# Optimization experiments

Measured on AMD Instinct MI355X. Metric: run time of the kernel, lower is better.

The kernel has to match this reference:

```python
import jax, jax.numpy as jnp
import numpy as np
from jax import lax

N_NODES = 4096
WINDOW = 288
SLIDE = 12
ENC_STEPS = 12
DEC_STEPS = 12
HID = 64
EMB = 64
PRED = 12
C1, C2 = 32, 64
KSZ, STR = 10, 2
OUT_LEN = 66  # ((288-10)//2+1 -> 140; (140-10)//2+1 -> 66)
EPS = 1e-5


def _conv1d(x, w, b, stride):
    # x: [N, Cin, L], w: [Cout, Cin, K]
    y = lax.conv_general_dilated(x, w, (stride,), 'VALID',
                                 dimension_numbers=('NCH', 'OIH', 'NCH'))
    return y + b[None, :, None]


def _bn(x, g, b):
    # BatchNorm1d training-mode stats over (batch, length) per channel
    m = x.mean(axis=(0, 2), keepdims=True)
    v = x.var(axis=(0, 2), keepdims=True)
    return (x - m) * jax.lax.rsqrt(v + EPS) * g[None, :, None] + b[None, :, None]


def _embed(x, conv1_w, conv1_b, conv2_w, conv2_b, bn1_g, bn1_b, bn2_g, bn2_b,
           fcconv_w, fcconv_b, fc_w, fc_b):
    # x: [N, WINDOW] -> [N, EMB]
    x = x[:, None, :]                                   # [N,1,W]
    x = _bn(jax.nn.relu(_conv1d(x, conv1_w, conv1_b, STR)), bn1_g, bn1_b)
    x = _bn(jax.nn.relu(_conv1d(x, conv2_w, conv2_b, STR)), bn2_g, bn2_b)
    x = jax.nn.relu(_conv1d(x, fcconv_w, fcconv_b, 1))  # [N,1,OUT_LEN]
    x = jnp.einsum('ncl,le->nce', x, fc_w) + fc_b       # [N,1,EMB]
    # NOTE: original code calls F.relu(x) but discards the result -> no relu here
    return x[:, 0, :]


def _gconv(x, adj, W, b):
    # diffusion conv: [x, A x, 2A(Ax) - x] (K=2, includes identity term)
    x1 = adj @ x
    x2 = 2.0 * (adj @ x1) - x
    return jnp.concatenate([x, x1, x2], axis=-1) @ W + b


def _dcgru_cell(x, h, adj, Wg, bg, Wc, bc):
    ru = jax.nn.sigmoid(_gconv(jnp.concatenate([x, h], -1), adj, Wg, bg))
    r, u = jnp.split(ru, 2, axis=-1)
    c = jnp.tanh(_gconv(jnp.concatenate([x, r * h], -1), adj, Wc, bc))
    return u * h + (1.0 - u) * c


def setup_inputs() -> dict:
    key = jax.random.key(0)
    ks = jax.random.split(key, 20)
    n_mat = 3  # K+1 diffusion matrices
    gin = (EMB + HID) * n_mat
    inp = {
        'inputs': jax.random.normal(ks[0], (N_NODES, (ENC_STEPS + DEC_STEPS - 1) * SLIDE + WINDOW), jnp.float32),
        'targets': jax.random.normal(ks[1], (N_NODES, DEC_STEPS * PRED), jnp.float32),
        'conv1_w': jax.random.normal(ks[3], (C1, 1, KSZ), jnp.float32) * 0.1,
        'conv1_b': jnp.zeros((C1,), jnp.float32),
        'conv2_w': jax.random.normal(ks[4], (C2, C1, KSZ), jnp.float32) * 0.1,
        'conv2_b': jnp.zeros((C2,), jnp.float32),
        'bn1_g': jnp.ones((C1,), jnp.float32), 'bn1_b': jnp.zeros((C1,), jnp.float32),
        'bn2_g': jnp.ones((C2,), jnp.float32), 'bn2_b': jnp.zeros((C2,), jnp.float32),
        'fcconv_w': jax.random.normal(ks[5], (1, C2, 1), jnp.float32) * 0.1,
        'fcconv_b': jnp.zeros((1,), jnp.float32),
        'fc_w': jax.random.normal(ks[6], (OUT_LEN, EMB), jnp.float32) * (1.0 / np.sqrt(OUT_LEN)),
        'fc_b': jnp.zeros((EMB,), jnp.float32),
        'enc_Wg': jax.random.normal(ks[7], (gin, 2 * HID), jnp.float32) * (1.0 / np.sqrt(gin)),
        'enc_bg': jnp.ones((2 * HID,), jnp.float32),
        'enc_Wc': jax.random.normal(ks[8], (gin, HID), jnp.float32) * (1.0 / np.sqrt(gin)),
        'enc_bc': jnp.zeros((HID,), jnp.float32),
        'dec_Wg': jax.random.normal(ks[9], (gin, 2 * HID), jnp.float32) * (1.0 / np.sqrt(gin)),
        'dec_bg': jnp.ones((2 * HID,), jnp.float32),
        'dec_Wc': jax.random.normal(ks[10], (gin, HID), jnp.float32) * (1.0 / np.sqrt(gin)),
        'dec_bc': jnp.zeros((HID,), jnp.float32),
        'pred_w': jax.random.normal(ks[11], (HID, PRED), jnp.float32) * (1.0 / np.sqrt(HID)),
        'pred_b': jnp.full((PRED,), 0.1, jnp.float32),
    }
    a = jax.random.uniform(ks[2], (N_NODES, N_NODES), jnp.float32)
    inp['adj'] = a / a.sum(axis=-1, keepdims=True)  # row-stochastic adjacency
    return inp


def reference(inputs, targets, adj,
              conv1_w, conv1_b, conv2_w, conv2_b, bn1_g, bn1_b, bn2_g, bn2_b,
              fcconv_w, fcconv_b, fc_w, fc_b,
              enc_Wg, enc_bg, enc_Wc, enc_bc,
              dec_Wg, dec_bg, dec_Wc, dec_bc,
              pred_w, pred_b):
    n = inputs.shape[0]
    # windowed views: idx[i] = i*SLIDE, 24 windows of length WINDOW
    idx = SLIDE * jnp.arange(ENC_STEPS + DEC_STEPS)
    wins = inputs[:, idx[:, None] + jnp.arange(WINDOW)]        # [N, 24, W]
    wins = jnp.transpose(wins, (1, 0, 2))                      # [24, N, W]
    embs = jax.vmap(lambda w: _embed(w, conv1_w, conv1_b, conv2_w, conv2_b,
                                     bn1_g, bn1_b, bn2_g, bn2_b,
                                     fcconv_w, fcconv_b, fc_w, fc_b))(wins)  # [24,N,EMB]
    enc_x, dec_x = embs[:ENC_STEPS], embs[ENC_STEPS:]

    h0 = jnp.zeros((n, HID), inputs.dtype)
    def enc_step(h, x):
        return _dcgru_cell(x, h, adj, enc_Wg, enc_bg, enc_Wc, enc_bc), None
    h_enc, _ = lax.scan(enc_step, h0, enc_x)

    # decoder: each step uses the SAME encoder hidden state (as in original code)
    dec_h = jax.vmap(lambda x: _dcgru_cell(x, h_enc, adj, dec_Wg, dec_bg, dec_Wc, dec_bc))(dec_x)  # [12,N,HID]
    preds = dec_h @ pred_w + pred_b                             # [12,N,PRED]
    return jnp.transpose(preds, (1, 0, 2)).reshape(n, DEC_STEPS * PRED)
```

## Files before the change

### kernel.cpp

```cpp
#include <hip/hip_runtime.h>
#include <hip/hip_bf16.h>
#include <math.h>

#define NN     4096
#define INLEN  564
#define NT     24
#define NC1    32
#define NC2    64
#define KS     10
#define EPS    1e-5f

typedef short s8v __attribute__((ext_vector_type(8)));
typedef short s4v __attribute__((ext_vector_type(4)));
typedef float f4v __attribute__((ext_vector_type(4)));
typedef float f2v __attribute__((ext_vector_type(2)));

static const long O_COLS   = 0;
static const long O_COLSQ  = 8960;
static const long O_STATS  = 17920;
static const long O_H      = 20992;
static const long ZERO_FLOATS = 291328;
static const long O_A1     = 291328;
static const long O_D1     = 292096;
static const long O_CB2    = 292864;
static const long O_W2B    = 532480;
static const long O_G1P    = 778240;
static const long O_Y2     = 19128320;
static const long O_EMBS   = 28041216;
static const long O_ADJB   = 532480;
static const long O_PP     = 8921088;
static const long O_X      = 13115392;
static const long O_T1     = 13901824;
static const long O_T1T    = 14426112;
static const long O_T2     = 14688256;
static const long O_RH     = 15212544;
static const long O_RHT    = 15474688;
static const long O_P1S    = 15605760;
static const long O_P1ST   = 15867904;
static const long O_P2S    = 15998976;
static const long O_UE     = 16261120;
static const long O_X12    = 16392192;
static const long O_XT12   = 22683648;
static const long O_EB     = 16392192;
static const long O_EBT    = 20062208;
static const long O_AE1    = 21897216;
static const long O_AE1T   = 25567232;
static const long O_AE2    = 27795456;
static const long O_RHB    = 31465472;
static const long O_P1B    = 34611200;
static const long O_P1BT   = O_PP;
static const long O_P2B    = O_X;
static const long O_HD     = O_PP;

struct Src { const float* p; int ld; int off; int tmul; };

static __device__ __forceinline__ float cvt_bf(short s) {
  return __uint_as_float(((unsigned)(unsigned short)s) << 16);
}
static __device__ __forceinline__ short bf16bits(float v) {
  __hip_bfloat16_raw r = __hip_bfloat16_raw(__float2bfloat16(v));
  return (short)r.x;
}

__global__ __launch_bounds__(256) void k_conv1n(const float* __restrict__ inp,
    const float* __restrict__ w1, const float* __restrict__ b1,
    __hip_bfloat16* __restrict__ g1p) {
  __shared__ float xin[INLEN];
  __shared__ float wl[320];
  __shared__ float bl[32];
  int n = blockIdx.x, tid = threadIdx.x;
  for (int i=tid; i<INLEN; i+=256) xin[i] = inp[(long)n*INLEN + i];
  for (int i=tid; i<320; i+=256) wl[i] = w1[i];
  if (tid < 32)  bl[tid] = b1[tid];
  __syncthreads();
  int c = tid & 31, pb = tid >> 5;
  float wreg[KS];
  #pragma unroll
  for (int k=0;k<KS;k++) wreg[k] = wl[c*KS+k];
  float bias = bl[c];
  for (int p = pb; p < 280; p += 8) {
    float acc = 0.f;
    if (p < 278) {
      acc = bias;
      #pragma unroll
      for (int k=0;k<KS;k++) acc = fmaf(wreg[k], xin[2*p+k], acc);
      acc = fmaxf(acc, 0.f);
    }
    g1p[((long)n*280 + p)*32 + c] = __float2bfloat16(acc);
  }
}

__global__ __launch_bounds__(256) void k_colsum2(const __hip_bfloat16* __restrict__ g1p,
    float* __restrict__ colS, float* __restrict__ colSQ) {
  int gid = blockIdx.x*256 + threadIdx.x;
  int cg = gid % 1120, chunk = gid / 1120;
  int col0 = cg*8;
  float s[8], sq[8];
  #pragma unroll
  for (int j=0;j<8;j++) { s[j]=0.f; sq[j]=0.f; }
  int n0 = chunk*128;
  const short* gp = (const short*)g1p;
  for (int n=n0; n<n0+128; n++) {
    s8v v = *(const s8v*)(gp + (long)n*8960 + col0);
    #pragma unroll
    for (int j=0;j<8;j++) { float f = cvt_bf(v[j]); s[j]+=f; sq[j]+=f*f; }
  }
  #pragma unroll
  for (int j=0;j<8;j++) { atomicAdd(&colS[col0+j], s[j]); atomicAdd(&colSQ[col0+j], sq[j]); }
}

__global__ __launch_bounds__(64) void k_bn1aff(const float* __restrict__ colS,
    const float* __restrict__ colSQ, const float* __restrict__ g, const float* __restrict__ b,
    float* __restrict__ a1, float* __restrict__ d1) {
  int i = blockIdx.x*64 + threadIdx.x;
  if (i >= NT*NC1) return;
  int t = i / NC1, c = i % NC1;
  float s=0.f, sq=0.f;
  for (int p=6*t; p<6*t+140; p++) { s += colS[p*32+c]; sq += colSQ[p*32+c]; }
  float cnt = 4096.f*140.f;
  float m = s/cnt;
  float v = sq/cnt - m*m;
  float a = g[c]*rsqrtf(v+EPS);
  a1[i] = a;
  d1[i] = b[c] - m*a;
}

__global__ __launch_bounds__(256) void k_w2b(const float* __restrict__ w2,
    const float* __restrict__ b2, const float* __restrict__ a1, const float* __restrict__ d1,
    __hip_bfloat16* __restrict__ w2b, float* __restrict__ cb2) {
  int i = blockIdx.x*256 + threadIdx.x;
  if (i >= NT*NC2) return;
  int t = i>>6, c2 = i&63;
  float cb = b2[c2];
  for (int c1=0;c1<NC1;c1++) {
    float a = a1[t*32+c1], d = d1[t*32+c1];
    float wsum = 0.f;
    for (int k=0;k<KS;k++) {
      float wv = w2[(c2*32+c1)*KS+k];
      wsum += wv;
      w2b[(((long)t*10 + k)*64 + c2)*32 + c1] = __float2bfloat16(wv*a);
    }
    cb += wsum*d;
  }
  cb2[i] = cb;
}

__global__ __launch_bounds__(256) void k_conv2m(const __hip_bfloat16* __restrict__ g1p,
    const __hip_bfloat16* __restrict__ w2b, const float* __restrict__ cb2,
    __hip_bfloat16* __restrict__ y2, float* __restrict__ stats, int t) {
  __shared__ __attribute__((aligned(16))) short patch[4*140*40];
  __shared__ float sS[64], sQ[64];
  int tid = threadIdx.x, w = tid>>6, lane = tid&63;
  int n0 = blockIdx.x*4;
  if (tid < 64) { sS[tid]=0.f; sQ[tid]=0.f; }
  const short* gp = (const short*)g1p;
  for (int f = tid; f < 2240; f += 256) {
    int nn = f / 560, rr = f % 560;
    int row = rr >> 2, kq = rr & 3;
    s8v v = *(const s8v*)(gp + ((long)(n0+nn)*280 + 6*t + row)*32 + kq*8);
    *(s8v*)&patch[(nn*140 + row)*40 + kq*8] = v;
  }
  __syncthreads();
  int q = lane>>4, m = lane&15;
  f4v acc[5][4];
  #pragma unroll
  for (int a=0;a<5;a++)
    #pragma unroll
    for (int b=0;b<4;b++) acc[a][b] = (f4v){0.f,0.f,0.f,0.f};
  const short* wb = (const short*)w2b + (long)t*10*64*32;
  for (int s=0; s<10; s++) {
    int j = s>>1, r = s&1;
    s8v bfr[4];
    #pragma unroll
    for (int ng=0; ng<4; ng++)
      bfr[ng] = *(const s8v*)(wb + (long)(s*64 + ng*16 + m)*32 + q*8);
    #pragma unroll
    for (int mg=0; mg<5; mg++) {
      int l2 = mg*16 + m;
      int u = l2 + j; u = (u>69)?69:u;
      s8v afr = *(const s8v*)&patch[(w*140 + 2*u + r)*40 + q*8];
      #pragma unroll
      for (int ng=0; ng<4; ng++)
        acc[mg][ng] = __builtin_amdgcn_mfma_f32_16x16x32_bf16(afr, bfr[ng], acc[mg][ng], 0,0,0);
    }
  }
  int node = n0 + w;
  float s1a[4]={0,0,0,0}, s2a[4]={0,0,0,0};
  #pragma unroll
  for (int mg=0; mg<5; mg++) {
    int l2b = mg*16 + q*4;
    #pragma unroll
    for (int ng=0; ng<4; ng++) {
      int c2 = ng*16 + m;
      float cbv = cb2[t*64 + c2];
      float vv[4];
      #pragma unroll
      for (int rr=0; rr<4; rr++) {
        float v = fmaxf(acc[mg][ng][rr] + cbv, 0.f);
        vv[rr] = v;
        if (l2b + rr < 66) { s1a[ng] += v; s2a[ng] += v*v; }
      }
      long base = ((long)node*64 + c2)*68 + l2b;
      if (mg < 4) {
        s4v o;
        #pragma unroll
        for (int rr=0; rr<4; rr++) o[rr] = bf16bits(vv[rr]);
        *(s4v*)((short*)y2 + base) = o;
      } else {
        for (int rr=0; rr<4; rr++) if (l2b+rr < 66) y2[base+rr] = __float2bfloat16(vv[rr]);
      }
    }
  }
  #pragma unroll
  for (int ng=0; ng<4; ng++) {
    atomicAdd(&sS[ng*16+m], s1a[ng]);
    atomicAdd(&sQ[ng*16+m], s2a[ng]);
  }
  __syncthreads();
  if (tid < 64) {
    atomicAdd(&stats[t*128+tid], sS[tid]);
    atomicAdd(&stats[t*128+64+tid], sQ[tid]);
  }
}

__global__ __launch_bounds__(256) void k_pass2(const __hip_bfloat16* __restrict__ y2,
    const float* __restrict__ stats, const float* __restrict__ bn2g, const float* __restrict__ bn2b,
    const float* __restrict__ fcvw, const float* __restrict__ fcvb,
    const float* __restrict__ fcW, const float* __restrict__ fcB,
    float* __restrict__ embs, int t) {
  __shared__ __attribute__((aligned(16))) short yb[4*64*68];
  __shared__ float fw[66*64];
  __shared__ float fwa[64], cfcs[64];
  __shared__ float zbuf[4][68];
  int tid = threadIdx.x;
  int n0 = blockIdx.x*4;
  const short* yg = (const short*)y2;
  for (int f=tid; f<2176; f+=256)
    *(s8v*)&yb[f*8] = *(const s8v*)(yg + (long)n0*64*68 + f*8);
  for (int i=tid; i<66*64; i+=256) fw[i] = fcW[i];
  if (tid < 64) {
    float cnt = 4096.f*66.f;
    float m = stats[t*128+tid]/cnt;
    float v = stats[t*128+64+tid]/cnt - m*m;
    float a = bn2g[tid]*rsqrtf(v+EPS);
    float d = bn2b[tid] - m*a;
    fwa[tid]  = fcvw[tid]*a;
    cfcs[tid] = fcvw[tid]*d;
  }
  __syncthreads();
  float cfc = fcvb[0];
  #pragma unroll 8
  for (int c=0;c<64;c++) cfc += cfcs[c];
  for (int idx=tid; idx<4*66; idx+=256) {
    int nn = idx/66, l = idx%66;
    float z = cfc;
    #pragma unroll 8
    for (int c=0;c<64;c++) z = fmaf(fwa[c], cvt_bf(yb[(nn*64+c)*68 + l]), z);
    zbuf[nn][l] = fmaxf(z, 0.f);
  }
  __syncthreads();
  int nn = tid>>6, e = tid&63;
  float acc = fcB[e];
  for (int l=0;l<66;l++) acc = fmaf(zbuf[nn][l], fw[l*64+e], acc);
  embs[((long)t*NN + n0+nn)*64 + e] = acc;
}

__global__ __launch_bounds__(256) void k_cvtadj(const float* __restrict__ adj,
    __hip_bfloat16* __restrict__ adjb) {
  long gid = ((long)blockIdx.x*256 + threadIdx.x)*4;
  float4 v = *(const float4*)(adj + gid);
  adjb[gid+0] = __float2bfloat16(v.x);
  adjb[gid+1] = __float2bfloat16(v.y);
  adjb[gid+2] = __float2bfloat16(v.z);
  adjb[gid+3] = __float2bfloat16(v.w);
}

template<int BN>
__global__ __launch_bounds__(256) void k_mmb(const __hip_bfloat16* __restrict__ A,
    const __hip_bfloat16* __restrict__ Bt, float* __restrict__ P,
    int N, int kchunk, long zoff,
    float* __restrict__ dst, const float* __restrict__ ref,
    __hip_bfloat16* __restrict__ dstT, int mode, int writeT, int zsplit) {
  constexpr int BM = 64;
  constexpr int WN = BN/2;
  constexpr int MI = 2;
  constexpr int NJ = WN/16;
  constexpr int AIT = 2;
  constexpr int BIT = BN*8/256;
  __shared__ __attribute__((aligned(16))) short As[BM*64];
  __shared__ __attribute__((aligned(16))) short Bs[BN*64];
  int tid = threadIdx.x;
  int w = tid >> 6, lane = tid & 63;
  int wm = w >> 1, wn = w & 1;
  int q = lane >> 4, m = lane & 15;
  long Mb = (long)blockIdx.x * BM;
  int Nb = blockIdx.y * BN;
  int k0 = blockIdx.z * kchunk;
  const short* Ag = (const short*)A;
  const short* Bg = (const short*)Bt;
  s8v arA[AIT], brA[BIT], arB[AIT], brB[BIT];

  auto loadAr = [&](s8v* d, int kb){
    #pragma unroll
    for (int i2=0;i2<AIT;i2++){ int f=tid+i2*256; int kq=f&7, row=f>>3;
      d[i2] = *(const s8v*)(Ag + (Mb+row)*4096 + kb + kq*8); } };
  auto loadBr = [&](s8v* d, int kb){
    #pragma unroll
    for (int i2=0;i2<BIT;i2++){ int f=tid+i2*256; int kq=f&7, col=f>>3;
      d[i2] = *(const s8v*)(Bg + (long)(Nb+col)*4096 + kb + kq*8); } };

  f4v acc[MI][NJ];
  #pragma unroll
  for (int i=0;i<MI;i++)
    #pragma unroll
    for (int j=0;j<NJ;j++) acc[i][j] = (f4v){0.f,0.f,0.f,0.f};

  auto writeS = [&](s8v* a, s8v* b){
    #pragma unroll
    for (int i2=0;i2<AIT;i2++){ int f=tid+i2*256; int kq=f&7, row=f>>3;
      *(s8v*)&As[(row*8 + (kq ^ (row&7)))*8] = a[i2]; }
    #pragma unroll
    for (int i2=0;i2<BIT;i2++){ int f=tid+i2*256; int kq=f&7, col=f>>3;
      *(s8v*)&Bs[(col*8 + (kq ^ (col&7)))*8] = b[i2]; } };
  auto compute = [&](){
    #pragma unroll
    for (int h2=0; h2<2; ++h2) {
      s8v af[MI], bfv[NJ];
      #pragma unroll
      for (int i=0;i<MI;i++) {
        int row = wm*32 + i*16 + m;
        af[i] = *(const s8v*)&As[(row*8 + ((h2*4+q) ^ (row&7)))*8];
      }
      #pragma unroll
      for (int j=0;j<NJ;j++) {
        int col = wn*WN + j*16 + m;
        bfv[j] = *(const s8v*)&Bs[(col*8 + ((h2*4+q) ^ (col&7)))*8];
      }
      #pragma unroll
      for (int i=0;i<MI;i++)
        #pragma unroll
        for (int j=0;j<NJ;j++)
          acc[i][j] = __builtin_amdgcn_mfma_f32_16x16x32_bf16(af[i], bfv[j], acc[i][j], 0, 0, 0);
    } };

  loadAr(arA, k0);      loadBr(brA, k0);
  loadAr(arB, k0+64);   loadBr(brB, k0+64);
  int kiters = kchunk >> 6;
  for (int it = 0; it < kiters; it += 2) {
    __syncthreads();
    writeS(arA, brA);
    __syncthreads();
    { int kn = (it+2 < kiters) ? k0 + (it+2)*64 : k0;
      loadAr(arA, kn); loadBr(brA, kn); }
    compute();
    __syncthreads();
    writeS(arB, brB);
    __syncthreads();
    { int kn = (it+3 < kiters) ? k0 + (it+3)*64 : k0;
      loadAr(arB, kn); loadBr(brB, kn); }
    compute();
  }

  if (zsplit > 1) {
    float* pp = P + (long)blockIdx.z * zoff;
    #pragma unroll
    for (int i=0;i<MI;i++) {
      long row0 = Mb + wm*32 + i*16 + q*4;
      #pragma unroll
      for (int j=0;j<NJ;j++) {
        int col = Nb + wn*WN + j*16 + m;
        #pragma unroll
        for (int r=0;r<4;r++) pp[(row0+r)*N + col] = acc[i][j][r];
      }
    }
  } else {
    #pragma unroll
    for (int i=0;i<MI;i++) {
      long row0 = Mb + wm*32 + i*16 + q*4;
      #pragma unroll
      for (int j=0;j<NJ;j++) {
        int col = Nb + wn*WN + j*16 + m;
        float vr[4];
        #pragma unroll
        for (int r=0;r<4;r++) {
          long idx = (row0+r)*N + col;
          float v = acc[i][j][r];
          if (mode) v = 2.f*v - ref[idx];
          dst[idx] = v;
          vr[r] = v;
        }
        if (writeT) {
          s4v o;
          #pragma unroll
          for (int r=0;r<4;r++) o[r] = bf16bits(vr[r]);
          *(s4v*)((short*)dstT + (long)col*4096 + row0) = o;
        }
      }
    }
  }
}

__global__ __launch_bounds__(256) void k_redT(const float* __restrict__ P,
    float* __restrict__ dst, const float* __restrict__ ref,
    __hip_bfloat16* __restrict__ dstT, int ldc, int ksplit, long zoff, int mode,
    int writeF, int writeT) {
  __shared__ float tile[64][65];
  int tid = threadIdx.x;
  int n0 = blockIdx.x*64, c0 = blockIdx.y*64;
  for (int i=0; i<16; i++) {
    int flat = i*256 + tid;
    int cc = flat & 63, nn = flat >> 6;
    long idx = (long)(n0+nn)*ldc + c0+cc;
    float v = P[idx];
    for (int s=1; s<ksplit; s++) v += P[(long)s*zoff + idx];
    if (mode) v = 2.f*v - ref[idx];
    if (writeF) dst[idx] = v;
    tile[nn][cc] = v;
  }
  __syncthreads();
  if (writeT) {
    for (int i=0; i<16; i++) {
      int flat = i*256 + tid;
      int nn = flat & 63, cc = flat >> 6;
      dstT[(long)(c0+cc)*4096 + n0+nn] = __float2bfloat16(tile[nn][cc]);
    }
  }
}

__global__ __launch_bounds__(256) void k_prepX(const float* __restrict__ embs,
    float* __restrict__ X12, __hip_bfloat16* __restrict__ Xt12) {
  __shared__ float tile[64][65];
  int tid = threadIdx.x;
  int n0 = blockIdx.x*64, c0 = blockIdx.y*64, t = blockIdx.z;
  float* X = X12 + (long)t*524288;
  __hip_bfloat16* Xt = Xt12 + (long)t*524288;
  for (int i=0; i<16; i++) {
    int flat = i*256 + tid;
    int cc = flat & 63, nn = flat >> 6;
    int col = c0 + cc, n = n0 + nn;
    float v = (col < 64) ? embs[((long)t*NN + n)*64 + col] : 0.f;
    X[(long)n*128 + col] = v;
    tile[nn][cc] = v;
  }
  __syncthreads();
  for (int i=0; i<16; i++) {
    int flat = i*256 + tid;
    int nn = flat & 63, cc = flat >> 6;
    Xt[(long)(c0+cc)*4096 + n0+nn] = __float2bfloat16(tile[nn][cc]);
  }
}

__global__ __launch_bounds__(256) void k_gatherE(const float* __restrict__ embs,
    const float* __restrict__ h, float* __restrict__ Eb, __hip_bfloat16* __restrict__ Ebt) {
  __shared__ float tile[64][65];
  int tid = threadIdx.x;
  int n0 = blockIdx.x*64, c0 = blockIdx.y*64;
  for (int i=0; i<16; i++) {
    int flat = i*256 + tid;
    int cc = flat & 63, nn = flat >> 6;
    int col = c0 + cc, n = n0 + nn;
    float v;
    if (col < 768)      v = embs[((long)(12 + (col>>6))*NN + n)*64 + (col & 63)];
    else if (col < 832) v = h[(long)n*64 + (col - 768)];
    else                v = 0.f;
    Eb[(long)n*896 + col] = v;
    tile[nn][cc] = v;
  }
  __syncthreads();
  for (int i=0; i<16; i++) {
    int flat = i*256 + tid;
    int nn = flat & 63, cc = flat >> 6;
    Ebt[(long)(c0+cc)*4096 + n0+nn] = __float2bfloat16(tile[nn][cc]);
  }
}

template<int RPT>
__global__ __launch_bounds__(256) void k_ggemm2(
    Src s0, Src s1, Src s2, Src s3, Src s4, Src s5,
    const float* __restrict__ W, const float* __restrict__ bias, int N, int mode,
    float* __restrict__ o1, int ld1, int t1, __hip_bfloat16* __restrict__ o1t,
    __hip_bfloat16* __restrict__ o2, const float* __restrict__ h,
    float* __restrict__ xnext, __hip_bfloat16* __restrict__ xtnext) {
  constexpr int BM = 16*RPT;
  __shared__ float Ags[32][BM+4];
  __shared__ float Bgs[32][68];
  int tid = threadIdx.x;
  long Mb = (long)blockIdx.x * BM;
  int Nb = blockIdx.y * 64;
  int tr = tid >> 4, tc = tid & 15;
  float acc[RPT][4];
  #pragma unroll
  for (int a=0;a<RPT;a++)
    #pragma unroll
    for (int b=0;b<4;b++) acc[a][b] = 0.f;
  float ar[2*RPT], br[8];
  auto pick = [&](int c)->Src {
    switch (c >> 1) {
      case 0: return s0; case 1: return s1; case 2: return s2;
      case 3: return s3; case 4: return s4; default: return s5;
    } };
  auto loadA = [&](int c){
    Src S = pick(c); int cc0 = (c & 1)*32;
    #pragma unroll
    for (int h0=0; h0<2*RPT; h0++) {
      int idx = tid + h0*256;
      int kk = idx & 31, mm = idx >> 5;
      long row = Mb + mm; int tt = (int)(row >> 12); int n = (int)(row & 4095);
      ar[h0] = S.p[(long)n*S.ld + S.off + S.tmul*(tt*64) + cc0 + kk];
    } };
  auto loadB = [&](int c){
    #pragma unroll
    for (int h0=0; h0<8; h0++) {
      int idx = tid + h0*256;
      int kk = idx >> 6, cc = idx & 63;
      br[h0] = W[(long)(c*32+kk)*N + Nb + cc];
    } };
  loadA(0); loadB(0);
  for (int c=0; c<12; c++) {
    __syncthreads();
    #pragma unroll
    for (int h0=0; h0<2*RPT; h0++) {
      int idx = tid + h0*256;
      int kk = idx & 31, mm = idx >> 5;
      int sw = (RPT >= 4) ? ((kk>>3)&3) : 0;
      Ags[kk][mm ^ sw] = ar[h0];
    }
    #pragma unroll
    for (int h0=0; h0<8; h0++)     { int idx = tid + h0*256; Bgs[idx >> 6][idx & 63] = br[h0]; }
    __syncthreads();
    if (c < 11) { loadA(c+1); loadB(c+1); }
    #pragma unroll
    for (int kk=0; kk<32; kk++) {
      f4v b4 = *(const f4v*)&Bgs[kk][tc*4];
      if constexpr (RPT == 4) {
        constexpr int dummy = 0; (void)dummy;
        f4v a0 = *(const f4v*)&Ags[kk][tr*4];
        const int s = (kk>>3)&3;
        #pragma unroll
        for (int rr=0; rr<4; rr++)
          #pragma unroll
          for (int j=0; j<4; j++)
            acc[rr][j] = fmaf(a0[rr ^ s], b4[j], acc[rr][j]);
      } else if constexpr (RPT == 2) {
        f2v a0 = *(const f2v*)&Ags[kk][tr*2];
        #pragma unroll
        for (int rr=0; rr<2; rr++)
          #pragma unroll
          for (int j=0; j<4; j++)
            acc[rr][j] = fmaf(a0[rr], b4[j], acc[rr][j]);
      } else {
        float a0 = Ags[kk][tr];
        #pragma unroll
        for (int j=0; j<4; j++)
          acc[0][j] = fmaf(a0, b4[j], acc[0][j]);
      }
    }
  }
  #pragma unroll
  for (int rr=0; rr<RPT; rr++) {
    long row = Mb + tr*RPT + rr;
    int tt = (int)(row >> 12); int n = (int)(row & 4095);
    #pragma unroll
    for (int j=0; j<4; j++) {
      int col = Nb + tc*4 + j;
      float g = acc[rr][j] + bias[col];
      if (mode == 0) {
        float sg = 1.f/(1.f + expf(-g));
        if (col < 64) {
          float v = sg * h[(long)n*64 + col];
          o1[(long)n*ld1 + (long)t1*tt*64 + col] = v;
          o1t[((long)t1*tt*64 + col)*4096 + n] = __float2bfloat16(v);
        } else {
          o2[(long)row*64 + (col - 64)] = __float2bfloat16(sg);
        }
      } else {
        float uu = __bfloat162float(o2[(long)row*64 + col]);
        float v = uu*h[(long)n*64 + col] + (1.f - uu)*tanhf(g);
        o1[(long)row*64 + col] = v;
        if (xnext) {
          xnext[(long)n*128 + 64 + col] = v;
          xtnext[(long)(64 + col)*4096 + n] = __float2bfloat16(v);
        }
      }
    }
  }
}

__global__ __launch_bounds__(256) void k_pred(const float* __restrict__ hd,
    const float* __restrict__ pw, const float* __restrict__ pb, float* __restrict__ out) {
  int gid = blockIdx.x*256 + threadIdx.x;
  int wid = gid >> 6;
  int lane = threadIdx.x & 63;
  if (wid >= 12*NN) return;
  int t = wid >> 12, n = wid & 4095;
  float hv = hd[(long)wid*64 + lane];
  float res = 0.f;
  #pragma unroll
  for (int p=0;p<12;p++) {
    float v = hv * pw[lane*12 + p];
    #pragma unroll
    for (int off=32; off>0; off>>=1) v += __shfl_xor(v, off, 64);
    if (lane == p) res = v + pb[p];
  }
  if (lane < 12) out[(long)n*144 + t*12 + lane] = res;
}

extern "C" void kernel_launch(void* const* d_in, const int* in_sizes, int n_in,
                              void* d_out, int out_size, void* d_ws, size_t ws_size,
                              hipStream_t stream) {
  const float* inp  = (const float*)d_in[0];
  const float* c1w  = (const float*)d_in[2];
  const float* c1b  = (const float*)d_in[3];
  const float* c2w  = (const float*)d_in[4];
  const float* c2b  = (const float*)d_in[5];
  const float* bn1g = (const float*)d_in[6];
  const float* bn1b = (const float*)d_in[7];
  const float* bn2g = (const float*)d_in[8];
  const float* bn2b = (const float*)d_in[9];
  const float* fcvw = (const float*)d_in[10];
  const float* fcvb = (const float*)d_in[11];
  const float* fcW  = (const float*)d_in[12];
  const float* fcB  = (const float*)d_in[13];
  const float* eWg  = (const float*)d_in[14];
  const float* ebg  = (const float*)d_in[15];
  const float* eWc  = (const float*)d_in[16];
  const float* ebc  = (const float*)d_in[17];
  const float* dWg  = (const float*)d_in[18];
  const float* dbg  = (const float*)d_in[19];
  const float* dWc  = (const float*)d_in[20];
  const float* dbc  = (const float*)d_in[21];
  const float* pw   = (const float*)d_in[22];
  const float* pb   = (const float*)d_in[23];
  const float* adj  = (const float*)d_in[n_in-1];
  for (int i=0;i<n_in;i++) if (in_sizes[i] == NN*NN) adj = (const float*)d_in[i];

  float* ws = (float*)d_ws;
  float* colS  = ws + O_COLS;
  float* colSQ = ws + O_COLSQ;
  float* stats = ws + O_STATS;
  float* h     = ws + O_H;
  float* a1    = ws + O_A1;
  float* d1    = ws + O_D1;
  float* cb2   = ws + O_CB2;
  __hip_bfloat16* w2b = (__hip_bfloat16*)(ws + O_W2B);
  __hip_bfloat16* g1p = (__hip_bfloat16*)(ws + O_G1P);
  __hip_bfloat16* y2  = (__hip_bfloat16*)(ws + O_Y2);
  float* embs  = ws + O_EMBS;
  __hip_bfloat16* adjb = (__hip_bfloat16*)(ws + O_ADJB);
  float* Pp    = ws + O_PP;
  float* T1    = ws + O_T1;
  __hip_bfloat16* T1t = (__hip_bfloat16*)(ws + O_T1T);
  float* T2    = ws + O_T2;
  float* rh    = ws + O_RH;
  __hip_bfloat16* rht = (__hip_bfloat16*)(ws + O_RHT);
  float* P1s   = ws + O_P1S;
  __hip_bfloat16* P1st = (__hip_bfloat16*)(ws + O_P1ST);
  float* P2s   = ws + O_P2S;
  __hip_bfloat16* ue  = (__hip_bfloat16*)(ws + O_UE);
  float* X12   = ws + O_X12;
  __hip_bfloat16* Xt12 = (__hip_bfloat16*)(ws + O_XT12);
  float* Eb    = ws + O_EB;
  __hip_bfloat16* Ebt = (__hip_bfloat16*)(ws + O_EBT);
  float* AE1   = ws + O_AE1;
  __hip_bfloat16* AE1t = (__hip_bfloat16*)(ws + O_AE1T);
  float* AE2   = ws + O_AE2;
  float* RHb   = ws + O_RHB;
  float* P1B   = ws + O_P1B;
  float* P2B   = ws + O_P2B;
  float* hd    = ws + O_HD;
  __hip_bfloat16* RHbt = Ebt;
  __hip_bfloat16* P1Bt = (__hip_bfloat16*)(ws + O_P1BT);
  __hip_bfloat16* ud   = AE1t;

  auto S = [](const float* p, int ld, int off, int tmul){ Src s; s.p=p; s.ld=ld; s.off=off; s.tmul=tmul; return s; };

  hipMemsetAsync(ws, 0, ZERO_FLOATS*sizeof(float), stream);

  k_conv1n<<<4096, 256, 0, stream>>>(inp, c1w, c1b, g1p);
  k_colsum2<<<140, 256, 0, stream>>>(g1p, colS, colSQ);
  k_bn1aff<<<12, 64, 0, stream>>>(colS, colSQ, bn1g, bn1b, a1, d1);
  k_w2b   <<<6, 256, 0, stream>>>(c2w, c2b, a1, d1, w2b, cb2);
  for (int t=0; t<NT; t++) {
    k_conv2m<<<1024, 256, 0, stream>>>(g1p, w2b, cb2, y2, stats, t);
    k_pass2 <<<1024, 256, 0, stream>>>(y2, stats, bn2g, bn2b, fcvw, fcvb, fcW, fcB, embs, t);
  }

  k_cvtadj<<<16384, 256, 0, stream>>>(adj, adjb);

  k_prepX<<<dim3(64,2,12), 256, 0, stream>>>(embs, X12, Xt12);
  for (int t=0; t<12; t++) {
    const float* et = embs + (long)t*NN*64;
    float* X_t = X12 + (long)t*524288;
    __hip_bfloat16* Xt_t = Xt12 + (long)t*524288;
    float* Xn  = (t < 11) ? X12 + (long)(t+1)*524288 : (float*)nullptr;
    __hip_bfloat16* Xtn = (t < 11) ? Xt12 + (long)(t+1)*524288 : (__hip_bfloat16*)nullptr;
    k_mmb<128><<<dim3(64,1,8), 256, 0, stream>>>(adjb, Xt_t, Pp, 128, 512, 4096L*128,
        (float*)nullptr, (const float*)nullptr, (__hip_bfloat16*)nullptr, 0, 0, 8);
    k_redT<<<dim3(64,2), 256, 0, stream>>>(Pp, T1, (const float*)nullptr, T1t,
        128, 8, 4096L*128, 0, 1, 1);
    k_mmb<128><<<dim3(64,1,8), 256, 0, stream>>>(adjb, T1t, Pp, 128, 512, 4096L*128,
        (float*)nullptr, (const float*)nullptr, (__hip_bfloat16*)nullptr, 0, 0, 8);
    k_redT<<<dim3(64,2), 256, 0, stream>>>(Pp, T2, X_t, (__hip_bfloat16*)nullptr,
        128, 8, 4096L*128, 1, 1, 0);
    k_ggemm2<2><<<dim3(128,2), 256, 0, stream>>>(
        S(X_t,128,0,0), S(X_t,128,64,0), S(T1,128,0,0), S(T1,128,64,0), S(T2,128,0,0), S(T2,128,64,0),
        eWg, ebg, 128, 0, rh, 64, 0, rht, ue, h, (float*)nullptr, (__hip_bfloat16*)nullptr);
    k_mmb<64><<<dim3(64,1,8), 256, 0, stream>>>(adjb, rht, Pp, 64, 512, 4096L*64,
        (float*)nullptr, (const float*)nullptr, (__hip_bfloat16*)nullptr, 0, 0, 8);
    k_redT<<<dim3(64,1), 256, 0, stream>>>(Pp, P1s, (const float*)nullptr, P1st,
        64, 8, 4096L*64, 0, 1, 1);
    k_mmb<64><<<dim3(64,1,8), 256, 0, stream>>>(adjb, P1st, Pp, 64, 512, 4096L*64,
        (float*)nullptr, (const float*)nullptr, (__hip_bfloat16*)nullptr, 0, 0, 8);
    k_redT<<<dim3(64,1), 256, 0, stream>>>(Pp, P2s, rh, (__hip_bfloat16*)nullptr,
        64, 8, 4096L*64, 1, 1, 0);
    k_ggemm2<1><<<dim3(256,1), 256, 0, stream>>>(
        S(et,64,0,0), S(rh,64,0,0), S(T1,128,0,0), S(P1s,64,0,0), S(T2,128,0,0), S(P2s,64,0,0),
        eWc, ebc, 64, 1, h, 0, 0, (__hip_bfloat16*)nullptr, ue, h, Xn, Xtn);
  }

  k_gatherE<<<dim3(64,14), 256, 0, stream>>>(embs, h, Eb, Ebt);
  k_mmb<128><<<dim3(64,7,1), 256, 0, stream>>>(adjb, Ebt, Pp, 896, 4096, 0,
      AE1, (const float*)nullptr, AE1t, 0, 1, 1);
  k_mmb<128><<<dim3(64,7,1), 256, 0, stream>>>(adjb, AE1t, Pp, 896, 4096, 0,
      AE2, Eb, (__hip_bfloat16*)nullptr, 1, 0, 1);
  k_ggemm2<4><<<dim3(768,2), 256, 0, stream>>>(
      S(Eb,896,0,1), S(Eb,896,768,0), S(AE1,896,0,1), S(AE1,896,768,0), S(AE2,896,0,1), S(AE2,896,768,0),
      dWg, dbg, 128, 0, RHb, 768, 1, RHbt, ud, h, (float*)nullptr, (__hip_bfloat16*)nullptr);
  k_mmb<128><<<dim3(64,6,1), 256, 0, stream>>>(adjb, RHbt, Pp, 768, 4096, 0,
      P1B, (const float*)nullptr, P1Bt, 0, 1, 1);
  k_mmb<128><<<dim3(64,6,1), 256, 0, stream>>>(adjb, P1Bt, Pp, 768, 4096, 0,
      P2B, RHb, (__hip_bfloat16*)nullptr, 1, 0, 1);
  k_ggemm2<4><<<dim3(768,1), 256, 0, stream>>>(
      S(Eb,896,0,1), S(RHb,768,0,1), S(AE1,896,0,1), S(P1B,768,0,1), S(AE2,896,0,1), S(P2B,768,0,1),
      dWc, dbc, 64, 1, hd, 0, 0, (__hip_bfloat16*)nullptr, ud, h, (float*)nullptr, (__hip_bfloat16*)nullptr);

  k_pred<<<12288, 256, 0, stream>>>(hd, pw, pb, (float*)d_out);
}
```

Before: 4.975 ms.

## Use bf16 MFMA GEMM kernel for decoder gate projections

Adds k_ggemm3, a 64x64-tile GEMM that converts fp32 activations and weights to bf16 in swizzled LDS and computes with 16x16x32 bf16 MFMA instructions. The two decoder gate/candidate projection launches switch from the scalar-FMA k_ggemm2<4> to this kernel, and the now-unused RPT==4 swizzle path is removed from k_ggemm2. The aim is to replace FP32 FMA work on the large decoder GEMMs with matrix-core throughput, at the cost of bf16 rounding of the inputs.

```diff
diff --git a/kernel.cpp b/kernel.cpp
--- a/kernel.cpp
+++ b/kernel.cpp
@@ -522,8 +522,7 @@
     for (int h0=0; h0<2*RPT; h0++) {
       int idx = tid + h0*256;
       int kk = idx & 31, mm = idx >> 5;
-      int sw = (RPT >= 4) ? ((kk>>3)&3) : 0;
-      Ags[kk][mm ^ sw] = ar[h0];
+      Ags[kk][mm] = ar[h0];
     }
     #pragma unroll
     for (int h0=0; h0<8; h0++)     { int idx = tid + h0*256; Bgs[idx >> 6][idx & 63] = br[h0]; }
@@ -532,16 +531,7 @@
     #pragma unroll
     for (int kk=0; kk<32; kk++) {
       f4v b4 = *(const f4v*)&Bgs[kk][tc*4];
-      if constexpr (RPT == 4) {
-        constexpr int dummy = 0; (void)dummy;
-        f4v a0 = *(const f4v*)&Ags[kk][tr*4];
-        const int s = (kk>>3)&3;
-        #pragma unroll
-        for (int rr=0; rr<4; rr++)
-          #pragma unroll
-          for (int j=0; j<4; j++)
-            acc[rr][j] = fmaf(a0[rr ^ s], b4[j], acc[rr][j]);
-      } else if constexpr (RPT == 2) {
+      if constexpr (RPT == 2) {
         f2v a0 = *(const f2v*)&Ags[kk][tr*2];
         #pragma unroll
         for (int rr=0; rr<2; rr++)
@@ -580,6 +570,102 @@
         if (xnext) {
           xnext[(long)n*128 + 64 + col] = v;
           xtnext[(long)(64 + col)*4096 + n] = __float2bfloat16(v);
+        }
+      }
+    }
+  }
+}
+
+__global__ __launch_bounds__(256) void k_ggemm3(
+    Src s0, Src s1, Src s2, Src s3, Src s4, Src s5,
+    const float* __restrict__ W, const float* __restrict__ bias, int N, int mode,
+    float* __restrict__ o1, int ld1, int t1, __hip_bfloat16* __restrict__ o1t,
+    __hip_bfloat16* __restrict__ o2, const float* __restrict__ h) {
+  __shared__ __attribute__((aligned(16))) short As[64*32];
+  __shared__ __attribute__((aligned(16))) short Bs[64*32];
+  int tid = threadIdx.x;
+  int w = tid >> 6, lane = tid & 63;
+  int wm = w >> 1, wn = w & 1;
+  int q = lane >> 4, m = lane & 15;
+  long Mb = (long)blockIdx.x * 64;
+  int Nb = blockIdx.y * 64;
+  int arow = tid >> 2, ag = tid & 3;
+  int bnn  = tid & 63, bg = tid >> 6;
+  auto pick = [&](int c)->Src {
+    switch (c >> 1) {
+      case 0: return s0; case 1: return s1; case 2: return s2;
+      case 3: return s3; case 4: return s4; default: return s5;
+    } };
+  f4v a0r, a1r; float wr[8];
+  auto loadA = [&](int c){
+    Src S = pick(c); int cc0 = (c & 1)*32;
+    long row = Mb + arow; int tt = (int)(row >> 12); int n = (int)(row & 4095);
+    const float* p = S.p + (long)n*S.ld + S.off + S.tmul*(tt*64) + cc0 + ag*8;
+    a0r = *(const f4v*)p; a1r = *(const f4v*)(p+4);
+  };
+  auto loadB = [&](int c){
+    #pragma unroll
+    for (int jj=0;jj<8;jj++) wr[jj] = W[(long)(c*32 + bg*8 + jj)*N + Nb + bnn];
+  };
+  f4v acc[2][2];
+  #pragma unroll
+  for (int i=0;i<2;i++)
+    #pragma unroll
+    for (int j=0;j<2;j++) acc[i][j] = (f4v){0.f,0.f,0.f,0.f};
+  loadA(0); loadB(0);
+  for (int c=0; c<12; c++) {
+    __syncthreads();
+    {
+      s8v va;
+      #pragma unroll
+      for (int jj=0;jj<4;jj++) { va[jj] = bf16bits(a0r[jj]); va[4+jj] = bf16bits(a1r[jj]); }
+      *(s8v*)&As[(arow*4 + (ag ^ (arow&3)))*8] = va;
+      s8v vb;
+      #pragma unroll
+      for (int jj=0;jj<8;jj++) vb[jj] = bf16bits(wr[jj]);
+      *(s8v*)&Bs[(bnn*4 + (bg ^ (bnn&3)))*8] = vb;
+    }
+    __syncthreads();
+    if (c < 11) { loadA(c+1); loadB(c+1); }
+    s8v af[2], bfv[2];
+    #pragma unroll
+    for (int i=0;i<2;i++) {
+      int row = wm*32 + i*16 + m;
+      af[i] = *(const s8v*)&As[(row*4 + (q ^ (row&3)))*8];
+    }
+    #pragma unroll
+    for (int j=0;j<2;j++) {
+      int col = wn*32 + j*16 + m;
+      bfv[j] = *(const s8v*)&Bs[(col*4 + (q ^ (col&3)))*8];
+    }
+    #pragma unroll
+    for (int i=0;i<2;i++)
+      #pragma unroll
+      for (int j=0;j<2;j++)
+        acc[i][j] = __builtin_amdgcn_mfma_f32_16x16x32_bf16(af[i], bfv[j], acc[i][j], 0, 0, 0);
+  }
+  #pragma unroll
+  for (int i=0;i<2;i++) {
+    #pragma unroll
+    for (int r=0;r<4;r++) {
+      long row = Mb + wm*32 + i*16 + q*4 + r;
+      int tt = (int)(row >> 12); int n = (int)(row & 4095);
+      #pragma unroll
+      for (int j=0;j<2;j++) {
+        int col = Nb + wn*32 + j*16 + m;
+        float g = acc[i][j][r] + bias[col];
+        if (mode == 0) {
+          float sg = 1.f/(1.f + expf(-g));
+          if (col < 64) {
+            float v = sg * h[(long)n*64 + col];
+            o1[(long)n*ld1 + (long)t1*tt*64 + col] = v;
+            o1t[((long)t1*tt*64 + col)*4096 + n] = __float2bfloat16(v);
+          } else {
+            o2[(long)row*64 + (col - 64)] = __float2bfloat16(sg);
+          }
+        } else {
+          float uu = __bfloat162float(o2[(long)row*64 + col]);
+          o1[(long)row*64 + col] = uu*h[(long)n*64 + col] + (1.f - uu)*tanhf(g);
         }
       }
     }
@@ -723,16 +809,16 @@
       AE1, (const float*)nullptr, AE1t, 0, 1, 1);
   k_mmb<128><<<dim3(64,7,1), 256, 0, stream>>>(adjb, AE1t, Pp, 896, 4096, 0,
       AE2, Eb, (__hip_bfloat16*)nullptr, 1, 0, 1);
-  k_ggemm2<4><<<dim3(768,2), 256, 0, stream>>>(
+  k_ggemm3<<<dim3(768,2), 256, 0, stream>>>(
       S(Eb,896,0,1), S(Eb,896,768,0), S(AE1,896,0,1), S(AE1,896,768,0), S(AE2,896,0,1), S(AE2,896,768,0),
-      dWg, dbg, 128, 0, RHb, 768, 1, RHbt, ud, h, (float*)nullptr, (__hip_bfloat16*)nullptr);
+      dWg, dbg, 128, 0, RHb, 768, 1, RHbt, ud, h);
   k_mmb<128><<<dim3(64,6,1), 256, 0, stream>>>(adjb, RHbt, Pp, 768, 4096, 0,
       P1B, (const float*)nullptr, P1Bt, 0, 1, 1);
   k_mmb<128><<<dim3(64,6,1), 256, 0, stream>>>(adjb, P1Bt, Pp, 768, 4096, 0,
       P2B, RHb, (__hip_bfloat16*)nullptr, 1, 0, 1);
-  k_ggemm2<4><<<dim3(768,1), 256, 0, stream>>>(
+  k_ggemm3<<<dim3(768,1), 256, 0, stream>>>(
       S(Eb,896,0,1), S(RHb,768,0,1), S(AE1,896,0,1), S(P1B,768,0,1), S(AE2,896,0,1), S(P2B,768,0,1),
-      dWc, dbc, 64, 1, hd, 0, 0, (__hip_bfloat16*)nullptr, ud, h, (float*)nullptr, (__hip_bfloat16*)nullptr);
+      dWc, dbc, 64, 1, hd, 0, 0, (__hip_bfloat16*)nullptr, ud, h);
 
   k_pred<<<12288, 256, 0, stream>>>(hd, pw, pb, (float*)d_out);
 }
```

New measurement: 4.922 ms. About the same (-1.1%).
